# Kernel optimization log

Measured on AMD Instinct MI355X. Metric: run time of the kernel, lower is better.

Reference implementation:

```python
import jax, jax.numpy as jnp
import numpy as np

DIM = 1024
DIM_HEAD = 64
HEADS = 16
INNER = DIM_HEAD * HEADS  # 1024
EPS = 1e-5


def layernorm(x, g, b):
    mu = jnp.mean(x, axis=-1, keepdims=True)
    var = jnp.var(x, axis=-1, keepdims=True)
    return (x - mu) * jax.lax.rsqrt(var + EPS) * g + b


def setup_inputs() -> dict:
    key = jax.random.key(0)
    ks = jax.random.split(key, 8)
    b, n_media, n_lat = 16, 4096, 64
    x = jax.random.normal(ks[0], (b, n_media, DIM), dtype=jnp.float32)
    latents = jax.random.normal(ks[1], (b, n_lat, DIM), dtype=jnp.float32)
    s = 0.02
    Wq = jax.random.normal(ks[2], (DIM, INNER), dtype=jnp.float32) * s
    Wkv = jax.random.normal(ks[3], (DIM, 2 * INNER), dtype=jnp.float32) * s
    Wout = jax.random.normal(ks[4], (INNER, DIM), dtype=jnp.float32) * s
    return {
        "x": x,
        "latents": latents,
        "g_media": jnp.ones((DIM,), jnp.float32),
        "b_media": jnp.zeros((DIM,), jnp.float32),
        "g_lat": jnp.ones((DIM,), jnp.float32),
        "b_lat": jnp.zeros((DIM,), jnp.float32),
        "Wq": Wq,
        "Wkv": Wkv,
        "Wout": Wout,
    }


def reference(x, latents, g_media, b_media, g_lat, b_lat, Wq, Wkv, Wout):
    h, d = HEADS, DIM_HEAD
    scale = d ** -0.5
    x = layernorm(x, g_media, b_media)
    latents = layernorm(latents, g_lat, b_lat)
    q = latents @ Wq                                  # [b, i, inner]
    kv_input = jnp.concatenate([x, latents], axis=1)  # [b, j, dim]
    kv = kv_input @ Wkv                               # [b, j, 2*inner]
    k, v = jnp.split(kv, 2, axis=-1)
    B = q.shape[0]
    q = q.reshape(B, -1, h, d).transpose(0, 2, 1, 3) * scale  # [b, h, i, d]
    k = k.reshape(B, -1, h, d).transpose(0, 2, 1, 3)          # [b, h, j, d]
    v = v.reshape(B, -1, h, d).transpose(0, 2, 1, 3)
    sim = jnp.einsum('bhid,bhjd->bhij', q, k)
    attn = jax.nn.softmax(sim, axis=-1)  # max-subtract handled internally
    out = jnp.einsum('bhij,bhjd->bhid', attn, v)
    out = out.transpose(0, 2, 1, 3).reshape(B, -1, h * d)
    return out @ Wout
```

## Files before the change

### kernel.cpp

```cpp
#include <hip/hip_runtime.h>
#include <cstdint>
#include <cstddef>

typedef short bf16x8 __attribute__((ext_vector_type(8)));
typedef float floatx4 __attribute__((ext_vector_type(4)));

__device__ __forceinline__ float b2f(short s) {
  union { float f; unsigned u; } v; v.u = ((unsigned)(unsigned short)s) << 16; return v.f;
}
__device__ __forceinline__ short f2b(float f) {
  union { float f; unsigned u; } v; v.f = f;
  unsigned r = v.u + 0x7fffu + ((v.u >> 16) & 1u);
  return (short)(r >> 16);
}

__device__ __forceinline__ void gld_lds16(const void* g, void* l) {
  __builtin_amdgcn_global_load_lds((const __attribute__((address_space(1))) void*)g,
                                   (__attribute__((address_space(3))) void*)l, 16, 0, 0);
}

__device__ __forceinline__ void row_load16(const void* p, size_t eoff, bool isf, float* f) {
  if (isf) {
    const float4* r4 = (const float4*)((const float*)p + eoff);
    float4 a = r4[0], b = r4[1], c = r4[2], d = r4[3];
    f[0] = a.x; f[1] = a.y; f[2] = a.z; f[3] = a.w;
    f[4] = b.x; f[5] = b.y; f[6] = b.z; f[7] = b.w;
    f[8] = c.x; f[9] = c.y; f[10] = c.z; f[11] = c.w;
    f[12] = d.x; f[13] = d.y; f[14] = d.z; f[15] = d.w;
  } else {
    const short* rp = (const short*)p + eoff;
    bf16x8 v0 = *(const bf16x8*)rp, v1 = *(const bf16x8*)(rp + 8);
    const short* s0 = (const short*)&v0;
    const short* s1 = (const short*)&v1;
#pragma unroll
    for (int e = 0; e < 8; ++e) { f[e] = b2f(s0[e]); f[8 + e] = b2f(s1[e]); }
  }
}

__device__ __forceinline__ bool inputs_are_f32(const unsigned* sent) {
  return sent[0] != 0x3F803F80u;
}

__global__ __launch_bounds__(256) void ln_x_kernel(const void* __restrict__ x,
    const void* __restrict__ g, const void* __restrict__ b,
    short* __restrict__ lnkv, const unsigned* __restrict__ sent) {
  bool isf = inputs_are_f32(sent);
  int lane = threadIdx.x & 63, wv = threadIdx.x >> 6;
  int row = blockIdx.x * 4 + wv;
  float f[16], gg[16], bb[16];
  row_load16(x, (size_t)row * 1024 + lane * 16, isf, f);
  float sum = 0.f, sq = 0.f;
#pragma unroll
  for (int e = 0; e < 16; ++e) { sum += f[e]; sq += f[e] * f[e]; }
#pragma unroll
  for (int m = 1; m <= 32; m <<= 1) { sum += __shfl_xor(sum, m); sq += __shfl_xor(sq, m); }
  float mean = sum * (1.f / 1024.f);
  float var = sq * (1.f / 1024.f) - mean * mean;
  float rstd = rsqrtf(var + 1e-5f);
  row_load16(g, (size_t)lane * 16, isf, gg);
  row_load16(b, (size_t)lane * 16, isf, bb);
  bf16x8 o0, o1; short* os0 = (short*)&o0; short* os1 = (short*)&o1;
#pragma unroll
  for (int e = 0; e < 8; ++e) {
    os0[e] = f2b((f[e] - mean) * rstd * gg[e] + bb[e]);
    os1[e] = f2b((f[8 + e] - mean) * rstd * gg[8 + e] + bb[8 + e]);
  }
  size_t orow = (size_t)(row >> 12) * 4160 + (row & 4095);
  short* op = lnkv + orow * 1024 + lane * 16;
  *(bf16x8*)op = o0; *(bf16x8*)(op + 8) = o1;
}

__global__ __launch_bounds__(256) void ln_lat_kernel(const void* __restrict__ lat,
    const void* __restrict__ g, const void* __restrict__ b,
    short* __restrict__ lnlat, short* __restrict__ lnkv,
    const unsigned* __restrict__ sent) {
  bool isf = inputs_are_f32(sent);
  int lane = threadIdx.x & 63, wv = threadIdx.x >> 6;
  int row = blockIdx.x * 4 + wv;
  float f[16], gg[16], bb[16];
  row_load16(lat, (size_t)row * 1024 + lane * 16, isf, f);
  float sum = 0.f, sq = 0.f;
#pragma unroll
  for (int e = 0; e < 16; ++e) { sum += f[e]; sq += f[e] * f[e]; }
#pragma unroll
  for (int m = 1; m <= 32; m <<= 1) { sum += __shfl_xor(sum, m); sq += __shfl_xor(sq, m); }
  float mean = sum * (1.f / 1024.f);
  float var = sq * (1.f / 1024.f) - mean * mean;
  float rstd = rsqrtf(var + 1e-5f);
  row_load16(g, (size_t)lane * 16, isf, gg);
  row_load16(b, (size_t)lane * 16, isf, bb);
  bf16x8 o0, o1; short* os0 = (short*)&o0; short* os1 = (short*)&o1;
#pragma unroll
  for (int e = 0; e < 8; ++e) {
    os0[e] = f2b((f[e] - mean) * rstd * gg[e] + bb[e]);
    os1[e] = f2b((f[8 + e] - mean) * rstd * gg[8 + e] + bb[8 + e]);
  }
  short* op1 = lnlat + (size_t)row * 1024 + lane * 16;
  *(bf16x8*)op1 = o0; *(bf16x8*)(op1 + 8) = o1;
  size_t orow = (size_t)(row >> 6) * 4160 + 4096 + (row & 63);
  short* op2 = lnkv + orow * 1024 + lane * 16;
  *(bf16x8*)op2 = o0; *(bf16x8*)(op2 + 8) = o1;
}

__global__ __launch_bounds__(256) void transpose_any(const void* __restrict__ in,
    short* __restrict__ out, int R, int C, const unsigned* __restrict__ sent) {
  bool isf = inputs_are_f32(sent);
  __shared__ short tile[32][33];
  int tx = threadIdx.x & 31, ty = threadIdx.x >> 5;
  int c0 = blockIdx.x * 32, r0 = blockIdx.y * 32;
#pragma unroll
  for (int i = 0; i < 32; i += 8) {
    size_t idx = (size_t)(r0 + ty + i) * C + c0 + tx;
    tile[ty + i][tx] = isf ? f2b(((const float*)in)[idx]) : ((const short*)in)[idx];
  }
  __syncthreads();
#pragma unroll
  for (int i = 0; i < 32; i += 8)
    out[(size_t)(c0 + ty + i) * R + r0 + tx] = tile[tx][ty + i];
}

__global__ __launch_bounds__(256) void gemm_bt(const short* __restrict__ A,
    const short* __restrict__ Bt, short* __restrict__ Cb, float* __restrict__ Cf,
    int M, int N, int K) {
  __shared__ short As[128][32];
  __shared__ short Bs[128][32];
  int tid = threadIdx.x;
  int wave = tid >> 6, lane = tid & 63;
  int quad = lane >> 4, l15 = lane & 15;
  int wm = (wave >> 1) * 64, wn = (wave & 1) * 64;
  size_t tm = (size_t)blockIdx.y * 128, tn = (size_t)blockIdx.x * 128;

  int srow = wave * 32 + (lane >> 2);
  int skoff = (((lane & 3) ^ ((lane >> 3) & 3)) * 8);
  const short* ga0 = A + (tm + srow) * (size_t)K + skoff;
  const short* ga1 = ga0 + (size_t)16 * K;
  const short* gb0 = Bt + (tn + srow) * (size_t)K + skoff;
  const short* gb1 = gb0 + (size_t)16 * K;
  char* la0 = (char*)(&As[0][0]) + (wave * 32) * 64;
  char* la1 = la0 + 16 * 64;
  char* lb0 = (char*)(&Bs[0][0]) + (wave * 32) * 64;
  char* lb1 = lb0 + 16 * 64;

  int swzr = ((l15 >> 1) & 3) * 16;

  floatx4 acc[4][4];
#pragma unroll
  for (int i = 0; i < 4; ++i)
#pragma unroll
    for (int j = 0; j < 4; ++j) acc[i][j] = (floatx4){0.f, 0.f, 0.f, 0.f};

  for (int k0 = 0; k0 < K; k0 += 32) {
    gld_lds16(ga0 + k0, la0);
    gld_lds16(ga1 + k0, la1);
    gld_lds16(gb0 + k0, lb0);
    gld_lds16(gb1 + k0, lb1);
    __syncthreads();
    bf16x8 af[4], bfv[4];
#pragma unroll
    for (int i = 0; i < 4; ++i)
      af[i] = *(const bf16x8*)((const char*)As + (wm + i * 16 + l15) * 64 + ((quad * 16) ^ swzr));
#pragma unroll
    for (int j = 0; j < 4; ++j)
      bfv[j] = *(const bf16x8*)((const char*)Bs + (wn + j * 16 + l15) * 64 + ((quad * 16) ^ swzr));
#pragma unroll
    for (int i = 0; i < 4; ++i)
#pragma unroll
      for (int j = 0; j < 4; ++j)
        acc[i][j] = __builtin_amdgcn_mfma_f32_16x16x32_bf16(af[i], bfv[j], acc[i][j], 0, 0, 0);
    __syncthreads();
  }

  if (Cf) {
#pragma unroll
    for (int i = 0; i < 4; ++i)
#pragma unroll
      for (int j = 0; j < 4; ++j)
#pragma unroll
        for (int r = 0; r < 4; ++r) {
          size_t m = tm + wm + i * 16 + quad * 4 + r;
          size_t n = tn + wn + j * 16 + l15;
          Cf[m * (size_t)N + n] = acc[i][j][r];
        }
  } else {
#pragma unroll
    for (int i = 0; i < 4; ++i)
#pragma unroll
      for (int j = 0; j < 4; ++j)
#pragma unroll
        for (int r = 0; r < 4; ++r) {
          size_t m = tm + wm + i * 16 + quad * 4 + r;
          size_t n = tn + wn + j * 16 + l15;
          Cb[m * (size_t)N + n] = f2b(acc[i][j][r]);
        }
  }
}

__global__ __launch_bounds__(256) void attn_kernel(const short* __restrict__ q,
    const short* __restrict__ kv, float* __restrict__ po,
    float* __restrict__ pm, float* __restrict__ pl) {
  __shared__ short Vt[64][32];
  __shared__ short Pl[4][16][32];

  int blk = blockIdx.x;
  int bh = blk >> 2, js = blk & 3;
  int b = bh >> 4, h = bh & 15;
  int tid = threadIdx.x;
  int w = tid >> 6, lane = tid & 63;
  int quad = lane >> 4, l15 = lane & 15;

  const short* qp = q + (size_t)(b * 64) * 1024 + h * 64;
  const short* kp = kv + (size_t)b * 4160 * 2048 + h * 64;
  const short* vp = kp + 1024;

  bf16x8 aq[2];
#pragma unroll
  for (int kh = 0; kh < 2; ++kh)
    aq[kh] = *(const bf16x8*)(qp + (size_t)(w * 16 + l15) * 1024 + kh * 32 + quad * 8);

  floatx4 o[4];
#pragma unroll
  for (int dt = 0; dt < 4; ++dt) o[dt] = (floatx4){0.f, 0.f, 0.f, 0.f};
  float mrun[4], lrun[4];
#pragma unroll
  for (int r = 0; r < 4; ++r) { mrun[r] = -1e30f; lrun[r] = 0.f; }

  const float scale = 0.125f;

  int vj = tid & 31;
  int vd0 = (tid >> 5) * 8;

  for (int t = js; t < 130; t += 4) {
    int j0 = t * 32;
    bf16x8 vv = *(const bf16x8*)(vp + (size_t)(j0 + vj) * 2048 + vd0);
    bf16x8 bk[2][2];
#pragma unroll
    for (int nt = 0; nt < 2; ++nt)
#pragma unroll
      for (int kh = 0; kh < 2; ++kh)
        bk[nt][kh] = *(const bf16x8*)(kp + (size_t)(j0 + nt * 16 + l15) * 2048 + kh * 32 + quad * 8);

    floatx4 z = (floatx4){0.f, 0.f, 0.f, 0.f};
    floatx4 s[2];
#pragma unroll
    for (int nt = 0; nt < 2; ++nt) {
      floatx4 a0 = __builtin_amdgcn_mfma_f32_16x16x32_bf16(aq[0], bk[nt][0], z, 0, 0, 0);
      s[nt] = __builtin_amdgcn_mfma_f32_16x16x32_bf16(aq[1], bk[nt][1], a0, 0, 0, 0);
    }

    {
      const short* vs = (const short*)&vv;
#pragma unroll
      for (int e = 0; e < 8; ++e) Vt[vd0 + e][vj] = vs[e];
    }

    float alpha[4];
#pragma unroll
    for (int r = 0; r < 4; ++r) {
      float v0 = s[0][r] * scale;
      float v1 = s[1][r] * scale;
      float tmx = fmaxf(v0, v1);
      tmx = fmaxf(tmx, __shfl_xor(tmx, 1));
      tmx = fmaxf(tmx, __shfl_xor(tmx, 2));
      tmx = fmaxf(tmx, __shfl_xor(tmx, 4));
      tmx = fmaxf(tmx, __shfl_xor(tmx, 8));
      float mn = fmaxf(mrun[r], tmx);
      float al = __expf(mrun[r] - mn);
      float p0 = __expf(v0 - mn);
      float p1 = __expf(v1 - mn);
      float ts = p0 + p1;
      ts += __shfl_xor(ts, 1);
      ts += __shfl_xor(ts, 2);
      ts += __shfl_xor(ts, 4);
      ts += __shfl_xor(ts, 8);
      lrun[r] = lrun[r] * al + ts;
      mrun[r] = mn;
      alpha[r] = al;
      int prow = quad * 4 + r;
      Pl[w][prow][l15] = f2b(p0);
      Pl[w][prow][16 + l15] = f2b(p1);
    }

#pragma unroll
    for (int dt = 0; dt < 4; ++dt)
#pragma unroll
      for (int r = 0; r < 4; ++r) o[dt][r] *= alpha[r];

    __syncthreads();

    bf16x8 aP = *(const bf16x8*)(&Pl[w][l15][0] + quad * 8);
    bf16x8 bV[4];
#pragma unroll
    for (int dt = 0; dt < 4; ++dt)
      bV[dt] = *(const bf16x8*)(&Vt[dt * 16 + l15][0] + quad * 8);
#pragma unroll
    for (int dt = 0; dt < 4; ++dt)
      o[dt] = __builtin_amdgcn_mfma_f32_16x16x32_bf16(aP, bV[dt], o[dt], 0, 0, 0);

    __syncthreads();
  }

  float* pob = po + (size_t)blk * 4096;
#pragma unroll
  for (int dt = 0; dt < 4; ++dt)
#pragma unroll
    for (int r = 0; r < 4; ++r)
      pob[(w * 16 + quad * 4 + r) * 64 + dt * 16 + l15] = o[dt][r];
  if (l15 == 0) {
#pragma unroll
    for (int r = 0; r < 4; ++r) {
      pm[(size_t)blk * 64 + w * 16 + quad * 4 + r] = mrun[r];
      pl[(size_t)blk * 64 + w * 16 + quad * 4 + r] = lrun[r];
    }
  }
}

__global__ __launch_bounds__(256) void attn_combine(const float* __restrict__ po,
    const float* __restrict__ pm, const float* __restrict__ pl,
    short* __restrict__ ao) {
  int bh = blockIdx.x;
  int b = bh >> 4, h = bh & 15;
  int tid = threadIdx.x;
  int i = tid >> 2;
  int cg = (tid & 3) * 16;
  size_t p0 = (size_t)bh * 4;
  float m0 = pm[(p0 + 0) * 64 + i], m1 = pm[(p0 + 1) * 64 + i];
  float m2 = pm[(p0 + 2) * 64 + i], m3 = pm[(p0 + 3) * 64 + i];
  float M = fmaxf(fmaxf(m0, m1), fmaxf(m2, m3));
  float w0 = __expf(m0 - M), w1 = __expf(m1 - M);
  float w2 = __expf(m2 - M), w3 = __expf(m3 - M);
  float den = pl[(p0 + 0) * 64 + i] * w0 + pl[(p0 + 1) * 64 + i] * w1 +
              pl[(p0 + 2) * 64 + i] * w2 + pl[(p0 + 3) * 64 + i] * w3;
  float rden = 1.f / den;
  const float* r0 = po + (p0 + 0) * 4096 + i * 64 + cg;
  const float* r1 = po + (p0 + 1) * 4096 + i * 64 + cg;
  const float* r2 = po + (p0 + 2) * 4096 + i * 64 + cg;
  const float* r3 = po + (p0 + 3) * 4096 + i * 64 + cg;
  short* op = ao + (size_t)(b * 64 + i) * 1024 + h * 64 + cg;
#pragma unroll
  for (int d = 0; d < 16; ++d) {
    float num = r0[d] * w0 + r1[d] * w1 + r2[d] * w2 + r3[d] * w3;
    op[d] = f2b(num * rden);
  }
}

extern "C" void kernel_launch(void* const* d_in, const int* in_sizes, int n_in,
                              void* d_out, int out_size, void* d_ws, size_t ws_size,
                              hipStream_t stream) {
  const void* x    = d_in[0];
  const void* lat  = d_in[1];
  const void* gm   = d_in[2];
  const void* bm   = d_in[3];
  const void* gl   = d_in[4];
  const void* bl   = d_in[5];
  const void* Wq   = d_in[6];
  const void* Wkv  = d_in[7];
  const void* Wout = d_in[8];
  const unsigned* sent = (const unsigned*)gm;

  char* ws = (char*)d_ws;
  size_t off = 0;
  auto alloc = [&](size_t bytes) { char* p = ws + off; off += (bytes + 255) & ~(size_t)255; return p; };
  short* kvb   = (short*)alloc((size_t)66560 * 2048 * 2);
  short* lnkv  = (short*)alloc((size_t)66560 * 1024 * 2);
  short* lnlat = (short*)alloc((size_t)1024 * 1024 * 2);
  short* qb    = (short*)alloc((size_t)1024 * 1024 * 2);
  short* ao    = (short*)alloc((size_t)1024 * 1024 * 2);
  short* WqT   = (short*)alloc((size_t)1024 * 1024 * 2);
  short* WkvT  = (short*)alloc((size_t)2048 * 1024 * 2);
  short* WoutT = (short*)alloc((size_t)1024 * 1024 * 2);
  float* po    = (float*)alloc((size_t)1024 * 4096 * 4);
  float* pm    = (float*)alloc((size_t)1024 * 64 * 4);
  float* pl    = (float*)alloc((size_t)1024 * 64 * 4);
  (void)in_sizes; (void)n_in; (void)out_size;

  if (off > ws_size) return;

  transpose_any<<<dim3(32, 32), 256, 0, stream>>>(Wq, WqT, 1024, 1024, sent);
  transpose_any<<<dim3(64, 32), 256, 0, stream>>>(Wkv, WkvT, 1024, 2048, sent);
  transpose_any<<<dim3(32, 32), 256, 0, stream>>>(Wout, WoutT, 1024, 1024, sent);
  ln_x_kernel<<<16384, 256, 0, stream>>>(x, gm, bm, lnkv, sent);
  ln_lat_kernel<<<256, 256, 0, stream>>>(lat, gl, bl, lnlat, lnkv, sent);
  gemm_bt<<<dim3(8, 8), 256, 0, stream>>>(lnlat, WqT, qb, nullptr, 1024, 1024, 1024);
  gemm_bt<<<dim3(16, 520), 256, 0, stream>>>(lnkv, WkvT, kvb, nullptr, 66560, 2048, 1024);
  attn_kernel<<<1024, 256, 0, stream>>>(qb, kvb, po, pm, pl);
  attn_combine<<<256, 256, 0, stream>>>(po, pm, pl, ao);
  gemm_bt<<<dim3(8, 8), 256, 0, stream>>>(ao, WoutT, nullptr, (float*)d_out, 1024, 1024, 1024);
}
```

Measured before the change: 962.4 us.

## Use 256x256-tile 8-wave GEMM with 4-stage LDS pipeline for KV projection

```diff
diff --git a/kernel.cpp b/kernel.cpp
--- a/kernel.cpp
+++ b/kernel.cpp
@@ -193,6 +193,119 @@
           Cb[m * (size_t)N + n] = f2b(acc[i][j][r]);
         }
   }
+}
+
+__global__ __launch_bounds__(512, 2) void gemm256_bt(const short* __restrict__ A,
+    const short* __restrict__ Bt, short* __restrict__ Cb, int M, int N, int K) {
+  __shared__ short lds[4][16384];
+  const int NT = K >> 5;
+
+  int tid = threadIdx.x;
+  int w = tid >> 6, lane = tid & 63;
+  int wr = w >> 2, wc = w & 3;
+  int quad = lane >> 4, l15 = lane & 15;
+
+  int ncol = N >> 8;
+  int nwg = gridDim.x * gridDim.y;
+  int L = blockIdx.y * gridDim.x + blockIdx.x;
+  int cpx = nwg >> 3;
+  int b = (L & 7) * cpx + (L >> 3);
+  int rowp = b / ncol;
+  int col = b - rowp * ncol;
+  size_t tm = (size_t)rowp * 256, tn = (size_t)col * 256;
+
+  int srow = w * 32 + (lane >> 2);
+  int schunk = ((lane & 3) ^ ((lane >> 3) & 3)) << 3;
+  const short* gA = A + (tm + srow) * (size_t)K + schunk;
+  const short* gB = Bt + (tn + srow) * (size_t)K + schunk;
+  size_t rstep = (size_t)16 * K;
+
+  floatx4 acc[8][4];
+#pragma unroll
+  for (int i = 0; i < 8; ++i)
+#pragma unroll
+    for (int j = 0; j < 4; ++j) acc[i][j] = (floatx4){0.f, 0.f, 0.f, 0.f};
+
+#pragma unroll
+  for (int pt = 0; pt < 3; ++pt) {
+    int kk = pt << 5;
+    char* lA = (char*)&lds[pt][0] + w * 2048;
+    char* lB = (char*)&lds[pt][8192] + w * 2048;
+    gld_lds16(gA + kk, lA);
+    gld_lds16(gA + kk + rstep, lA + 1024);
+    gld_lds16(gB + kk, lB);
+    gld_lds16(gB + kk + rstep, lB + 1024);
+  }
+  asm volatile("s_waitcnt vmcnt(8)" ::: "memory");
+  __builtin_amdgcn_s_barrier();
+  asm volatile("" ::: "memory");
+
+  int rsw = (quad ^ ((l15 >> 1) & 3)) << 4;
+  int arow0 = wr * 128 + l15;
+  int brow0 = wc * 64 + l15;
+
+  for (int t = 0; t < NT; ++t) {
+    int rb = t & 3, rs = (t + 3) & 3;
+    const char* As = (const char*)&lds[rb][0];
+    const char* Bs = (const char*)&lds[rb][8192];
+    bool st = (t + 3 < NT);
+    int k3 = (t + 3) << 5;
+    char* lA = (char*)&lds[rs][0] + w * 2048;
+    char* lB = (char*)&lds[rs][8192] + w * 2048;
+
+    bf16x8 af[4], bv[4];
+#pragma unroll
+    for (int i = 0; i < 4; ++i)
+      af[i] = *(const bf16x8*)(As + ((arow0 + i * 16) << 6) + rsw);
+#pragma unroll
+    for (int j = 0; j < 4; ++j)
+      bv[j] = *(const bf16x8*)(Bs + ((brow0 + j * 16) << 6) + rsw);
+    if (st) { gld_lds16(gA + k3, lA); gld_lds16(gA + k3 + rstep, lA + 1024); }
+    asm volatile("" ::: "memory");
+    __builtin_amdgcn_s_barrier();
+    asm volatile("s_waitcnt lgkmcnt(0)" ::: "memory");
+    __builtin_amdgcn_s_setprio(1);
+#pragma unroll
+    for (int i = 0; i < 4; ++i)
+#pragma unroll
+      for (int j = 0; j < 4; ++j)
+        acc[i][j] = __builtin_amdgcn_mfma_f32_16x16x32_bf16(af[i], bv[j], acc[i][j], 0, 0, 0);
+    __builtin_amdgcn_s_setprio(0);
+    asm volatile("" ::: "memory");
+    __builtin_amdgcn_s_barrier();
+    asm volatile("" ::: "memory");
+
+    bf16x8 ag[4];
+#pragma unroll
+    for (int i = 0; i < 4; ++i)
+      ag[i] = *(const bf16x8*)(As + ((arow0 + 64 + i * 16) << 6) + rsw);
+    if (st) { gld_lds16(gB + k3, lB); gld_lds16(gB + k3 + rstep, lB + 1024); }
+    if (t < NT - 3)       asm volatile("s_waitcnt vmcnt(8)" ::: "memory");
+    else if (t == NT - 3) asm volatile("s_waitcnt vmcnt(4)" ::: "memory");
+    else                  asm volatile("s_waitcnt vmcnt(0)" ::: "memory");
+    __builtin_amdgcn_s_barrier();
+    asm volatile("s_waitcnt lgkmcnt(0)" ::: "memory");
+    __builtin_amdgcn_s_setprio(1);
+#pragma unroll
+    for (int i = 0; i < 4; ++i)
+#pragma unroll
+      for (int j = 0; j < 4; ++j)
+        acc[4 + i][j] = __builtin_amdgcn_mfma_f32_16x16x32_bf16(ag[i], bv[j], acc[4 + i][j], 0, 0, 0);
+    __builtin_amdgcn_s_setprio(0);
+    asm volatile("" ::: "memory");
+    __builtin_amdgcn_s_barrier();
+    asm volatile("" ::: "memory");
+  }
+
+  size_t crow = tm + (size_t)wr * 128 + quad * 4;
+  size_t ccol = tn + (size_t)wc * 64 + l15;
+#pragma unroll
+  for (int i = 0; i < 8; ++i)
+#pragma unroll
+    for (int j = 0; j < 4; ++j)
+#pragma unroll
+      for (int r = 0; r < 4; ++r)
+        Cb[(crow + i * 16 + r) * (size_t)N + ccol + j * 16] = f2b(acc[i][j][r]);
 }
 
 __global__ __launch_bounds__(256) void attn_kernel(const short* __restrict__ q,
@@ -381,7 +494,7 @@
   ln_x_kernel<<<16384, 256, 0, stream>>>(x, gm, bm, lnkv, sent);
   ln_lat_kernel<<<256, 256, 0, stream>>>(lat, gl, bl, lnlat, lnkv, sent);
   gemm_bt<<<dim3(8, 8), 256, 0, stream>>>(lnlat, WqT, qb, nullptr, 1024, 1024, 1024);
-  gemm_bt<<<dim3(16, 520), 256, 0, stream>>>(lnkv, WkvT, kvb, nullptr, 66560, 2048, 1024);
+  gemm256_bt<<<dim3(8, 260), 512, 0, stream>>>(lnkv, WkvT, kvb, 66560, 2048, 1024);
   attn_kernel<<<1024, 256, 0, stream>>>(qb, kvb, po, pm, pl);
   attn_combine<<<256, 256, 0, stream>>>(po, pm, pl, ao);
   gemm_bt<<<dim3(8, 8), 256, 0, stream>>>(ao, WoutT, nullptr, (float*)d_out, 1024, 1024, 1024);
```

Measured after the change: 881.9 us. 1.09x faster.

## Add 128x256 double-buffered GEMM kernel for the large KV projection

Applied to the files above, without the earlier changes.

```diff
diff --git a/kernel.cpp b/kernel.cpp
--- a/kernel.cpp
+++ b/kernel.cpp
@@ -193,6 +193,90 @@
           Cb[m * (size_t)N + n] = f2b(acc[i][j][r]);
         }
   }
+}
+
+__global__ __launch_bounds__(512, 4) void gemm128x256_bt(const short* __restrict__ A,
+    const short* __restrict__ Bt, short* __restrict__ Cb, int M, int N, int K) {
+  __shared__ char lds[2][24576];
+  const int NT = K >> 5;
+
+  int tid = threadIdx.x;
+  int w = tid >> 6, lane = tid & 63;
+  int wr = w >> 2, wc = w & 3;
+  int quad = lane >> 4, l15 = lane & 15;
+
+  int ncol = N >> 8;
+  int nwg = gridDim.x * gridDim.y;
+  int L = blockIdx.y * gridDim.x + blockIdx.x;
+  int cpx = nwg >> 3;
+  int b = (L & 7) * cpx + (L >> 3);
+  int rowp = b / ncol;
+  int col = b - rowp * ncol;
+  size_t tm = (size_t)rowp * 128, tn = (size_t)col * 256;
+
+  int srow = tid >> 2;
+  int sc8 = (((tid & 3) ^ ((srow >> 1) & 3)) << 3);
+  const short* gA = A + (tm + srow) * (size_t)K + sc8;
+  const short* gB0 = Bt + (tn + srow) * (size_t)K + sc8;
+  const short* gB1 = gB0 + (size_t)128 * K;
+  char* dA = &lds[0][0] + (size_t)w * 1024;
+  char* dB0 = &lds[0][8192] + (size_t)w * 1024;
+  char* dB1 = dB0 + 8192;
+
+  floatx4 acc[4][4];
+#pragma unroll
+  for (int i = 0; i < 4; ++i)
+#pragma unroll
+    for (int j = 0; j < 4; ++j) acc[i][j] = (floatx4){0.f, 0.f, 0.f, 0.f};
+
+  gld_lds16(gA, dA);
+  gld_lds16(gB0, dB0);
+  gld_lds16(gB1, dB1);
+  asm volatile("s_waitcnt vmcnt(0)" ::: "memory");
+  __builtin_amdgcn_s_barrier();
+  asm volatile("" ::: "memory");
+
+  int rsw = (quad ^ ((l15 >> 1) & 3)) << 4;
+  int arow0 = wr * 64 + l15;
+  int brow0 = wc * 64 + l15;
+
+  for (int t = 0; t < NT; ++t) {
+    const char* S = lds[t & 1];
+    int so = ((t + 1) & 1) * 24576;
+    if (t + 1 < NT) {
+      int kk = (t + 1) << 5;
+      gld_lds16(gA + kk, dA + so);
+      gld_lds16(gB0 + kk, dB0 + so);
+      gld_lds16(gB1 + kk, dB1 + so);
+    }
+    bf16x8 af[4], bv[4];
+#pragma unroll
+    for (int i = 0; i < 4; ++i)
+      af[i] = *(const bf16x8*)(S + ((arow0 + i * 16) << 6) + rsw);
+#pragma unroll
+    for (int j = 0; j < 4; ++j)
+      bv[j] = *(const bf16x8*)(S + 8192 + ((brow0 + j * 16) << 6) + rsw);
+    __builtin_amdgcn_s_setprio(1);
+#pragma unroll
+    for (int i = 0; i < 4; ++i)
+#pragma unroll
+      for (int j = 0; j < 4; ++j)
+        acc[i][j] = __builtin_amdgcn_mfma_f32_16x16x32_bf16(af[i], bv[j], acc[i][j], 0, 0, 0);
+    __builtin_amdgcn_s_setprio(0);
+    asm volatile("s_waitcnt vmcnt(0)" ::: "memory");
+    __builtin_amdgcn_s_barrier();
+    asm volatile("" ::: "memory");
+  }
+
+  size_t crow = tm + (size_t)wr * 64 + quad * 4;
+  size_t ccol = tn + (size_t)wc * 64 + l15;
+#pragma unroll
+  for (int i = 0; i < 4; ++i)
+#pragma unroll
+    for (int j = 0; j < 4; ++j)
+#pragma unroll
+      for (int r = 0; r < 4; ++r)
+        Cb[(crow + i * 16 + r) * (size_t)N + ccol + j * 16] = f2b(acc[i][j][r]);
 }
 
 __global__ __launch_bounds__(256) void attn_kernel(const short* __restrict__ q,
@@ -381,7 +465,7 @@
   ln_x_kernel<<<16384, 256, 0, stream>>>(x, gm, bm, lnkv, sent);
   ln_lat_kernel<<<256, 256, 0, stream>>>(lat, gl, bl, lnlat, lnkv, sent);
   gemm_bt<<<dim3(8, 8), 256, 0, stream>>>(lnlat, WqT, qb, nullptr, 1024, 1024, 1024);
-  gemm_bt<<<dim3(16, 520), 256, 0, stream>>>(lnkv, WkvT, kvb, nullptr, 66560, 2048, 1024);
+  gemm128x256_bt<<<dim3(8, 520), 512, 0, stream>>>(lnkv, WkvT, kvb, 66560, 2048, 1024);
   attn_kernel<<<1024, 256, 0, stream>>>(qb, kvb, po, pm, pl);
   attn_combine<<<256, 256, 0, stream>>>(po, pm, pl, ao);
   gemm_bt<<<dim3(8, 8), 256, 0, stream>>>(ao, WoutT, nullptr, (float*)d_out, 1024, 1024, 1024);
```

Measured after the change: 861.5 us. -10.5%, faster.
